# Kernel optimization log

Measured on AMD Instinct MI355X. Metric: run time of the kernel, lower is better.

The kernel has to match this reference:

```python
import jax, jax.numpy as jnp
import numpy as np

OFFSET = 1.0
BANDWIDTH = 0.5
EPS = 1e-5


def _similarity(source, target):
    # source: [b, c, h, w] -> [b, ns, c]; target: [b, c, h2, w2] -> [b, nt, c]
    b, c = source.shape[0], source.shape[1]
    s = source.reshape(b, c, -1).transpose(0, 2, 1)                  # [b, ns, c]
    t = target.reshape(b, target.shape[1], -1).transpose(0, 2, 1)    # [b, nt, c]
    s_sqr = jnp.sum(s * s, axis=-1)                                  # [b, ns]
    t_sqr = jnp.sum(t * t, axis=-1)                                  # [b, nt]
    # pairwise squared distances [b, nt, ns]
    dist = t_sqr[:, :, None] - 2.0 * jnp.einsum('btc,bsc->bts', t, s) + s_sqr[:, None, :]
    dist = jnp.maximum(dist, 0.0)
    # per source-column min over target rows (chunking in torch is per-column, hence equivalent globally)
    min_dist = jnp.min(dist, axis=1, keepdims=True)                  # [b, 1, ns]
    sim = jnp.exp((OFFSET - dist / (min_dist + EPS)) / BANDWIDTH)    # [b, nt, ns]
    sim = sim / jnp.sum(sim, axis=1, keepdims=True)                  # column-normalize over target dim
    # max over source columns per target row, then mean over target rows
    return jnp.mean(jnp.max(sim, axis=2), axis=-1)                   # [b]


def _loss(source, target):
    return jnp.mean(-jnp.log(_similarity(source, target)))


def setup_inputs() -> dict:
    key = jax.random.key(0)
    k1, k2 = jax.random.split(key)
    source = jax.random.normal(k1, (2, 128, 64, 64), dtype=jnp.float32)
    target = jax.random.normal(k2, (2, 128, 64, 64), dtype=jnp.float32)
    return {"source": source, "target": target}


def reference(source, target):
    # is_symmetric=True, is_similarity=False -> symmetric loss
    return (_loss(source, target) + _loss(target, source)) / 2.0
```

## Files before the change

### kernel.cpp

```cpp
#include <hip/hip_runtime.h>
#include <math.h>

#define NB 2
#define NC 128
#define NN 4096
#define C2L 2.88539008177792681472f

typedef __attribute__((ext_vector_type(8))) short short8;
typedef __attribute__((ext_vector_type(4))) float f32x4;

__device__ unsigned short g_Tb[NB][NN][NC];
__device__ unsigned short g_Sb[NB][NN][NC];
__device__ float g_tsqr[NB][NN];
__device__ float g_ssqr[NB][NN];
__device__ float g_rowS[NB][NN];
__device__ float g_rowLZ[NB][NN];
__device__ float g_rowE[NB][NN];
__device__ float g_colS[NB][NN];
__device__ float g_colLZ[NB][NN];
__device__ float g_colE[NB][NN];
__device__ float g_colpart[NB][128][NN];
__device__ float g_rowpart[NB][16][NN];

#if __has_builtin(__builtin_amdgcn_exp2f)
__device__ __forceinline__ float fexp2(float x) { return __builtin_amdgcn_exp2f(x); }
#else
__device__ __forceinline__ float fexp2(float x) { return exp2f(x); }
#endif

#define GLL16(gsrc, ldst) \
  __builtin_amdgcn_global_load_lds((const __attribute__((address_space(1))) void*)(gsrc), \
                                   (__attribute__((address_space(3))) void*)(ldst), 16, 0, 0)

__device__ __forceinline__ unsigned f2bf(float f) {
    unsigned u = __float_as_uint(f);
    u += 0x7FFFu + ((u >> 16) & 1u);
    return u >> 16;
}

__global__ void __launch_bounds__(256) transpose_prep(const float* __restrict__ src,
                                                      const float* __restrict__ tgt) {
    __shared__ float ls[NC][68];
    __shared__ float redn[4][64];
    int bid = blockIdx.x;
    int mat = bid >> 7;
    int b   = (bid >> 6) & 1;
    int n0  = (bid & 63) << 6;
    int tid = threadIdx.x;
    const float* in = (mat ? tgt : src) + (size_t)b * NC * NN;
    unsigned short (*out)[NC] = mat ? g_Tb[b] : g_Sb[b];
    float* sq = mat ? g_tsqr[b] : g_ssqr[b];

    for (int idx = tid; idx < NC * 16; idx += 256) {
        int k = idx >> 4, c4 = (idx & 15) << 2;
        *(float4*)&ls[k][c4] = *(const float4*)(in + (size_t)k * NN + n0 + c4);
    }
    __syncthreads();
    {
        int n = tid & 63, c = tid >> 6;
        float psum = 0.f;
        for (int cc = c; cc < 16; cc += 4) {
            unsigned uo[4];
            #pragma unroll
            for (int e = 0; e < 4; ++e) {
                float v0 = ls[cc * 8 + 2 * e][n];
                float v1 = ls[cc * 8 + 2 * e + 1][n];
                psum = fmaf(v0, v0, psum);
                psum = fmaf(v1, v1, psum);
                uo[e] = f2bf(v0) | (f2bf(v1) << 16);
            }
            int swz = mat ? cc : (cc ^ (n & 7));
            *(uint4*)&out[n0 + n][swz * 8] = make_uint4(uo[0], uo[1], uo[2], uo[3]);
        }
        redn[c][n] = psum;
    }
    __syncthreads();
    if (tid < 64)
        sq[n0 + tid] = (redn[0][tid] + redn[1][tid]) + (redn[2][tid] + redn[3][tid]);
}

template<int PASS>
__global__ void __launch_bounds__(256) sweep_kernel() {
    __shared__ unsigned short Sp[256 * NC];

    int bid = blockIdx.x;
    int b   = bid >> 9;
    int st  = (bid >> 4) & 31;
    int pn  = bid & 15;
    int i0  = st * 128;
    int j0  = pn * 256;
    int tid = threadIdx.x;
    int w = tid >> 6, lane = tid & 63, q = lane >> 4, x = lane & 15;
    int iw = i0 + w * 32;

    #pragma unroll
    for (int it = 0; it < 16; ++it) {
        int l = tid + it * 256;
        GLL16(&g_Sb[b][j0 + (l >> 4)][(l & 15) * 8], &Sp[l * 8]);
    }

    short8 af[2][4];
    #pragma unroll
    for (int m = 0; m < 2; ++m)
        #pragma unroll
        for (int kk = 0; kk < 4; ++kk)
            af[m][kk] = *(const short8*)&g_Tb[b][iw + m * 16 + x][(kk * 4 + q) * 8];

    float tq[8], rS[8], rC[8];
    #pragma unroll
    for (int m = 0; m < 2; ++m)
        #pragma unroll
        for (int v = 0; v < 4; ++v) {
            int row = iw + m * 16 + q * 4 + v;
            tq[m * 4 + v] = g_tsqr[b][row];
            rS[m * 4 + v] = (PASS >= 2) ? g_rowS[b][row] : 0.f;
            rC[m * 4 + v] = (PASS == 3) ? (C2L - g_rowLZ[b][row]) : 0.f;
        }

    float sqc[4], cSc[4], cCc[4], sqn[4], cSn[4], cCn[4];
    #pragma unroll
    for (int n = 0; n < 4; ++n) {
        int col = j0 + n * 16 + x;
        sqn[n] = g_ssqr[b][col];
        cSn[n] = (PASS >= 2) ? g_colS[b][col] : 0.f;
        cCn[n] = (PASS == 3) ? (C2L - g_colLZ[b][col]) : 0.f;
    }

    float rstate[8];
    #pragma unroll
    for (int e = 0; e < 8; ++e)
        rstate[e] = (PASS == 1) ? 3.0e38f : (PASS == 2 ? 0.f : -3.0e38f);

    __syncthreads();

    for (int jt = 0; jt < 4; ++jt) {
        #pragma unroll
        for (int n = 0; n < 4; ++n) { sqc[n] = sqn[n]; cSc[n] = cSn[n]; cCc[n] = cCn[n]; }
        if (jt < 3) {
            #pragma unroll
            for (int n = 0; n < 4; ++n) {
                int col = j0 + (jt + 1) * 64 + n * 16 + x;
                sqn[n] = g_ssqr[b][col];
                if (PASS >= 2) cSn[n] = g_colS[b][col];
                if (PASS == 3) cCn[n] = C2L - g_colLZ[b][col];
            }
        }

        f32x4 acc[2][4];
        #pragma unroll
        for (int m = 0; m < 2; ++m)
            #pragma unroll
            for (int n = 0; n < 4; ++n)
                acc[m][n] = (f32x4){0.f, 0.f, 0.f, 0.f};

        #pragma unroll
        for (int kk = 0; kk < 4; ++kk) {
            short8 bf[4];
            #pragma unroll
            for (int n = 0; n < 4; ++n) {
                int r  = jt * 64 + n * 16 + x;
                int ch = (kk * 4 + q) ^ (r & 7);
                bf[n] = *(const short8*)&Sp[r * NC + ch * 8];
            }
            #pragma unroll
            for (int m = 0; m < 2; ++m)
                #pragma unroll
                for (int n = 0; n < 4; ++n)
                    acc[m][n] = __builtin_amdgcn_mfma_f32_16x16x32_bf16(af[m][kk], bf[n], acc[m][n], 0, 0, 0);
        }

        float cstate[4];
        #pragma unroll
        for (int n = 0; n < 4; ++n)
            cstate[n] = (PASS == 1) ? 3.0e38f : (PASS == 2 ? 0.f : -3.0e38f);

        #pragma unroll
        for (int m = 0; m < 2; ++m)
            #pragma unroll
            for (int n = 0; n < 4; ++n)
                #pragma unroll
                for (int v = 0; v < 4; ++v) {
                    float dv = fmaxf(fmaf(-2.f, acc[m][n][v], tq[m * 4 + v] + sqc[n]), 0.f);
                    if (PASS == 1) {
                        rstate[m * 4 + v] = fminf(rstate[m * 4 + v], dv);
                        cstate[n]         = fminf(cstate[n], dv);
                    } else if (PASS == 2) {
                        rstate[m * 4 + v] += fexp2(fmaf(dv, rS[m * 4 + v], C2L));
                        cstate[n]         += fexp2(fmaf(dv, cSc[n], C2L));
                    } else {
                        rstate[m * 4 + v] = fmaxf(rstate[m * 4 + v], fmaf(dv, cSc[n], cCc[n]));
                        cstate[n]         = fmaxf(cstate[n], fmaf(dv, rS[m * 4 + v], rC[m * 4 + v]));
                    }
                }

        #pragma unroll
        for (int off = 16; off < 64; off <<= 1)
            #pragma unroll
            for (int n = 0; n < 4; ++n) {
                float o = __shfl_xor(cstate[n], off);
                cstate[n] = (PASS == 1) ? fminf(cstate[n], o)
                           : (PASS == 2) ? cstate[n] + o : fmaxf(cstate[n], o);
            }
        if (q == 0)
            #pragma unroll
            for (int n = 0; n < 4; ++n)
                g_colpart[b][st * 4 + w][j0 + jt * 64 + n * 16 + x] = cstate[n];
    }

    #pragma unroll
    for (int off = 1; off < 16; off <<= 1)
        #pragma unroll
        for (int e = 0; e < 8; ++e) {
            float o = __shfl_xor(rstate[e], off);
            rstate[e] = (PASS == 1) ? fminf(rstate[e], o)
                       : (PASS == 2) ? rstate[e] + o : fmaxf(rstate[e], o);
        }
    if (x == 0)
        #pragma unroll
        for (int e = 0; e < 8; ++e)
            g_rowpart[b][pn][iw + (e >> 2) * 16 + q * 4 + (e & 3)] = rstate[e];
}

template<int PASS>
__global__ void __launch_bounds__(256) reduce_kernel() {
    int bid = blockIdx.x;
    int b = bid >> 8, g = bid & 255;
    int tid = threadIdx.x;
    int el = g * 16 + (tid >> 4);
    int part = tid & 15;

    float ca = (PASS == 1) ? 3.0e38f : (PASS == 2 ? 0.f : -3.0e38f);
    #pragma unroll
    for (int k = 0; k < 8; ++k) {
        float cv = g_colpart[b][part * 8 + k][el];
        if (PASS == 1) ca = fminf(ca, cv);
        else if (PASS == 2) ca += cv;
        else ca = fmaxf(ca, cv);
    }
    float ra = g_rowpart[b][part][el];

    #pragma unroll
    for (int off = 1; off < 16; off <<= 1) {
        float co = __shfl_xor(ca, off), ro = __shfl_xor(ra, off);
        if (PASS == 1) { ca = fminf(ca, co); ra = fminf(ra, ro); }
        else if (PASS == 2) { ca += co; ra += ro; }
        else { ca = fmaxf(ca, co); ra = fmaxf(ra, ro); }
    }
    if (part == 0) {
        if (PASS == 1) { g_colS[b][el] = -(C2L / (ca + 1e-5f)); g_rowS[b][el] = -(C2L / (ra + 1e-5f)); }
        if (PASS == 2) { g_colLZ[b][el] = log2f(ca);            g_rowLZ[b][el] = log2f(ra); }
        if (PASS == 3) { g_colE[b][el] = fexp2(ca);             g_rowE[b][el] = fexp2(ra); }
    }
}

__global__ void final_kernel(float* __restrict__ out) {
    int tid = threadIdx.x;
    float s[4] = {0.f, 0.f, 0.f, 0.f};
    for (int i = tid; i < NN; i += 256) {
        s[0] += g_rowE[0][i];
        s[1] += g_rowE[1][i];
        s[2] += g_colE[0][i];
        s[3] += g_colE[1][i];
    }
    __shared__ float red[4][4];
    int lane = tid & 63, w = tid >> 6;
    #pragma unroll
    for (int t = 0; t < 4; ++t) {
        float v = s[t];
        #pragma unroll
        for (int off = 32; off; off >>= 1) v += __shfl_down(v, off);
        if (lane == 0) red[t][w] = v;
    }
    __syncthreads();
    if (tid == 0) {
        float o = 0.f;
        #pragma unroll
        for (int t = 0; t < 4; ++t) {
            float S = red[t][0] + red[t][1] + red[t][2] + red[t][3];
            o += logf(S);
        }
        out[0] = logf((float)NN) - 0.25f * o;
    }
}

extern "C" void kernel_launch(void* const* d_in, const int* in_sizes, int n_in,
                              void* d_out, int out_size, void* d_ws, size_t ws_size,
                              hipStream_t stream) {
    const float* src = (const float*)d_in[0];
    const float* tgt = (const float*)d_in[1];
    (void)in_sizes; (void)n_in; (void)d_ws; (void)ws_size; (void)out_size;

    transpose_prep<<<256, 256, 0, stream>>>(src, tgt);
    sweep_kernel<1><<<1024, 256, 0, stream>>>();
    reduce_kernel<1><<<512, 256, 0, stream>>>();
    sweep_kernel<2><<<1024, 256, 0, stream>>>();
    reduce_kernel<2><<<512, 256, 0, stream>>>();
    sweep_kernel<3><<<1024, 256, 0, stream>>>();
    reduce_kernel<3><<<512, 256, 0, stream>>>();
    final_kernel<<<1, 256, 0, stream>>>((float*)d_out);
}
```

Baseline: 89.72 us.

## Double-buffer source tiles in LDS and widen sweep blocks to 512 columns

Each sweep block now covers 512 source columns instead of 256, staged as four 128-row chunks in two LDS buffers. The next chunk is prefetched asynchronously while the current one is consumed. This halves the grid to 512 blocks and halves the row partials per element, and the reduce kernel pads the missing 8 row partials with the identity value. The aim is to overlap global-to-LDS loads with MFMA work and to cut redundant T-fragment loads and partial-writing overhead, at the cost of fewer blocks (512 over 256 CUs) and an extra barrier per chunk.

```diff
diff --git a/kernel.cpp b/kernel.cpp
--- a/kernel.cpp
+++ b/kernel.cpp
@@ -81,22 +81,22 @@
 
 template<int PASS>
 __global__ void __launch_bounds__(256) sweep_kernel() {
-    __shared__ unsigned short Sp[256 * NC];
+    __shared__ unsigned short Sp[2][128 * NC];
 
     int bid = blockIdx.x;
-    int b   = bid >> 9;
-    int st  = (bid >> 4) & 31;
-    int pn  = bid & 15;
+    int b   = bid >> 8;
+    int st  = (bid >> 3) & 31;
+    int pn  = bid & 7;
     int i0  = st * 128;
-    int j0  = pn * 256;
+    int j0  = pn * 512;
     int tid = threadIdx.x;
     int w = tid >> 6, lane = tid & 63, q = lane >> 4, x = lane & 15;
     int iw = i0 + w * 32;
 
     #pragma unroll
-    for (int it = 0; it < 16; ++it) {
+    for (int it = 0; it < 8; ++it) {
         int l = tid + it * 256;
-        GLL16(&g_Sb[b][j0 + (l >> 4)][(l & 15) * 8], &Sp[l * 8]);
+        GLL16(&g_Sb[b][j0 + (l >> 4)][(l & 15) * 8], &Sp[0][l * 8]);
     }
 
     short8 af[2][4];
@@ -133,78 +133,93 @@
 
     __syncthreads();
 
-    for (int jt = 0; jt < 4; ++jt) {
-        #pragma unroll
-        for (int n = 0; n < 4; ++n) { sqc[n] = sqn[n]; cSc[n] = cSn[n]; cCc[n] = cCn[n]; }
-        if (jt < 3) {
-            #pragma unroll
-            for (int n = 0; n < 4; ++n) {
-                int col = j0 + (jt + 1) * 64 + n * 16 + x;
-                sqn[n] = g_ssqr[b][col];
-                if (PASS >= 2) cSn[n] = g_colS[b][col];
-                if (PASS == 3) cCn[n] = C2L - g_colLZ[b][col];
+    for (int p = 0; p < 4; ++p) {
+        if (p < 3) {
+            #pragma unroll
+            for (int it = 0; it < 8; ++it) {
+                int l = tid + it * 256;
+                GLL16(&g_Sb[b][j0 + (p + 1) * 128 + (l >> 4)][(l & 15) * 8],
+                      &Sp[(p + 1) & 1][l * 8]);
             }
         }
 
-        f32x4 acc[2][4];
-        #pragma unroll
-        for (int m = 0; m < 2; ++m)
+        #pragma unroll
+        for (int jt = 0; jt < 2; ++jt) {
+            int t = p * 2 + jt;
+            #pragma unroll
+            for (int n = 0; n < 4; ++n) { sqc[n] = sqn[n]; cSc[n] = cSn[n]; cCc[n] = cCn[n]; }
+            if (t < 7) {
+                #pragma unroll
+                for (int n = 0; n < 4; ++n) {
+                    int col = j0 + (t + 1) * 64 + n * 16 + x;
+                    sqn[n] = g_ssqr[b][col];
+                    if (PASS >= 2) cSn[n] = g_colS[b][col];
+                    if (PASS == 3) cCn[n] = C2L - g_colLZ[b][col];
+                }
+            }
+
+            f32x4 acc[2][4];
+            #pragma unroll
+            for (int m = 0; m < 2; ++m)
+                #pragma unroll
+                for (int n = 0; n < 4; ++n)
+                    acc[m][n] = (f32x4){0.f, 0.f, 0.f, 0.f};
+
+            #pragma unroll
+            for (int kk = 0; kk < 4; ++kk) {
+                short8 bf[4];
+                #pragma unroll
+                for (int n = 0; n < 4; ++n) {
+                    int r  = jt * 64 + n * 16 + x;
+                    int ch = (kk * 4 + q) ^ (r & 7);
+                    bf[n] = *(const short8*)&Sp[p & 1][r * NC + ch * 8];
+                }
+                #pragma unroll
+                for (int m = 0; m < 2; ++m)
+                    #pragma unroll
+                    for (int n = 0; n < 4; ++n)
+                        acc[m][n] = __builtin_amdgcn_mfma_f32_16x16x32_bf16(af[m][kk], bf[n], acc[m][n], 0, 0, 0);
+            }
+
+            float cstate[4];
             #pragma unroll
             for (int n = 0; n < 4; ++n)
-                acc[m][n] = (f32x4){0.f, 0.f, 0.f, 0.f};
-
-        #pragma unroll
-        for (int kk = 0; kk < 4; ++kk) {
-            short8 bf[4];
-            #pragma unroll
-            for (int n = 0; n < 4; ++n) {
-                int r  = jt * 64 + n * 16 + x;
-                int ch = (kk * 4 + q) ^ (r & 7);
-                bf[n] = *(const short8*)&Sp[r * NC + ch * 8];
-            }
+                cstate[n] = (PASS == 1) ? 3.0e38f : (PASS == 2 ? 0.f : -3.0e38f);
+
             #pragma unroll
             for (int m = 0; m < 2; ++m)
                 #pragma unroll
                 for (int n = 0; n < 4; ++n)
-                    acc[m][n] = __builtin_amdgcn_mfma_f32_16x16x32_bf16(af[m][kk], bf[n], acc[m][n], 0, 0, 0);
-        }
-
-        float cstate[4];
-        #pragma unroll
-        for (int n = 0; n < 4; ++n)
-            cstate[n] = (PASS == 1) ? 3.0e38f : (PASS == 2 ? 0.f : -3.0e38f);
-
-        #pragma unroll
-        for (int m = 0; m < 2; ++m)
-            #pragma unroll
-            for (int n = 0; n < 4; ++n)
-                #pragma unroll
-                for (int v = 0; v < 4; ++v) {
-                    float dv = fmaxf(fmaf(-2.f, acc[m][n][v], tq[m * 4 + v] + sqc[n]), 0.f);
-                    if (PASS == 1) {
-                        rstate[m * 4 + v] = fminf(rstate[m * 4 + v], dv);
-                        cstate[n]         = fminf(cstate[n], dv);
-                    } else if (PASS == 2) {
-                        rstate[m * 4 + v] += fexp2(fmaf(dv, rS[m * 4 + v], C2L));
-                        cstate[n]         += fexp2(fmaf(dv, cSc[n], C2L));
-                    } else {
-                        rstate[m * 4 + v] = fmaxf(rstate[m * 4 + v], fmaf(dv, cSc[n], cCc[n]));
-                        cstate[n]         = fmaxf(cstate[n], fmaf(dv, rS[m * 4 + v], rC[m * 4 + v]));
+                    #pragma unroll
+                    for (int v = 0; v < 4; ++v) {
+                        float dv = fmaxf(fmaf(-2.f, acc[m][n][v], tq[m * 4 + v] + sqc[n]), 0.f);
+                        if (PASS == 1) {
+                            rstate[m * 4 + v] = fminf(rstate[m * 4 + v], dv);
+                            cstate[n]         = fminf(cstate[n], dv);
+                        } else if (PASS == 2) {
+                            rstate[m * 4 + v] += fexp2(fmaf(dv, rS[m * 4 + v], C2L));
+                            cstate[n]         += fexp2(fmaf(dv, cSc[n], C2L));
+                        } else {
+                            rstate[m * 4 + v] = fmaxf(rstate[m * 4 + v], fmaf(dv, cSc[n], cCc[n]));
+                            cstate[n]         = fmaxf(cstate[n], fmaf(dv, rS[m * 4 + v], rC[m * 4 + v]));
+                        }
                     }
+
+            #pragma unroll
+            for (int off = 16; off < 64; off <<= 1)
+                #pragma unroll
+                for (int n = 0; n < 4; ++n) {
+                    float o = __shfl_xor(cstate[n], off);
+                    cstate[n] = (PASS == 1) ? fminf(cstate[n], o)
+                               : (PASS == 2) ? cstate[n] + o : fmaxf(cstate[n], o);
                 }
-
-        #pragma unroll
-        for (int off = 16; off < 64; off <<= 1)
-            #pragma unroll
-            for (int n = 0; n < 4; ++n) {
-                float o = __shfl_xor(cstate[n], off);
-                cstate[n] = (PASS == 1) ? fminf(cstate[n], o)
-                           : (PASS == 2) ? cstate[n] + o : fmaxf(cstate[n], o);
-            }
-        if (q == 0)
-            #pragma unroll
-            for (int n = 0; n < 4; ++n)
-                g_colpart[b][st * 4 + w][j0 + jt * 64 + n * 16 + x] = cstate[n];
+            if (q == 0)
+                #pragma unroll
+                for (int n = 0; n < 4; ++n)
+                    g_colpart[b][st * 4 + w][j0 + t * 64 + n * 16 + x] = cstate[n];
+        }
+
+        __syncthreads();
     }
 
     #pragma unroll
@@ -228,8 +243,9 @@
     int tid = threadIdx.x;
     int el = g * 16 + (tid >> 4);
     int part = tid & 15;
-
-    float ca = (PASS == 1) ? 3.0e38f : (PASS == 2 ? 0.f : -3.0e38f);
+    float ident = (PASS == 1) ? 3.0e38f : (PASS == 2 ? 0.f : -3.0e38f);
+
+    float ca = ident;
     #pragma unroll
     for (int k = 0; k < 8; ++k) {
         float cv = g_colpart[b][part * 8 + k][el];
@@ -237,7 +253,7 @@
         else if (PASS == 2) ca += cv;
         else ca = fmaxf(ca, cv);
     }
-    float ra = g_rowpart[b][part][el];
+    float ra = (part < 8) ? g_rowpart[b][part][el] : ident;
 
     #pragma unroll
     for (int off = 1; off < 16; off <<= 1) {
@@ -291,11 +307,11 @@
     (void)in_sizes; (void)n_in; (void)d_ws; (void)ws_size; (void)out_size;
 
     transpose_prep<<<256, 256, 0, stream>>>(src, tgt);
-    sweep_kernel<1><<<1024, 256, 0, stream>>>();
+    sweep_kernel<1><<<512, 256, 0, stream>>>();
     reduce_kernel<1><<<512, 256, 0, stream>>>();
-    sweep_kernel<2><<<1024, 256, 0, stream>>>();
+    sweep_kernel<2><<<512, 256, 0, stream>>>();
     reduce_kernel<2><<<512, 256, 0, stream>>>();
-    sweep_kernel<3><<<1024, 256, 0, stream>>>();
+    sweep_kernel<3><<<512, 256, 0, stream>>>();
     reduce_kernel<3><<<512, 256, 0, stream>>>();
     final_kernel<<<1, 256, 0, stream>>>((float*)d_out);
 }
```

Result: slower. 92.35 us (+2.9%).
